# Optimization experiments

Measured on AMD Instinct MI355X. Metric: run time of the kernel, lower is better.

Reference implementation:

```python
import jax, jax.numpy as jnp
import numpy as np

N, M, E, B = 50000, 4, 400000, 64
NHID, EMBED, NOUT, NLAYER = 64, 64, 1, 3


def _glorot(k, shape):
    fan_in = shape[0]
    return jax.random.normal(k, shape, jnp.float32) / np.float32(np.sqrt(fan_in))


def setup_inputs() -> dict:
    key = jax.random.key(0)
    ks = jax.random.split(key, 18)
    inp = {
        "additional_x": jax.random.normal(ks[0], (N, M, 1), jnp.float32),
        "edge_index": jax.random.randint(ks[1], (2, E), 0, N, dtype=jnp.int32),
        "batch": jnp.sort(jax.random.randint(ks[2], (N,), 0, B, dtype=jnp.int32)),
        # conv layer 0: in_channels=1, layers 1,2: in_channels=NHID (bias=False since bn='BN')
        "Wself0": _glorot(ks[3], (1, NHID)),
        "Wnei0": _glorot(ks[4], (1, NHID)),
        "Wself1": _glorot(ks[5], (NHID, NHID)),
        "Wnei1": _glorot(ks[6], (NHID, NHID)),
        "Wself2": _glorot(ks[7], (NHID, NHID)),
        "Wnei2": _glorot(ks[8], (NHID, NHID)),
        # inter_encoder: MLP(nlayer*nhid -> nhid -> nhid -> EMBED), no norm, relu between
        "W1": _glorot(ks[9], (NLAYER * NHID, NHID)),
        "b1": jnp.zeros((NHID,), jnp.float32),
        "W2": _glorot(ks[10], (NHID, NHID)),
        "b2": jnp.zeros((NHID,), jnp.float32),
        "W3": _glorot(ks[11], (NHID, EMBED)),
        "b3": jnp.zeros((EMBED,), jnp.float32),
        # output_encoder: single Linear (with_final_activation=False)
        "Wo": _glorot(ks[12], (EMBED, NOUT)),
        "bo": jnp.zeros((NOUT,), jnp.float32),
    }
    return inp


def reference(additional_x, edge_index, batch,
              Wself0, Wnei0, Wself1, Wnei1, Wself2, Wnei2,
              W1, b1, W2, b2, W3, b3, Wo, bo):
    src, dst = edge_index[0], edge_index[1]

    def conv(x, Ws, Wn):
        # GraphConv: W_self x_i + W_neigh * sum_{j in N(i)} x_j   (x: [N, M, Din])
        agg = jax.ops.segment_sum(x[src], dst, num_segments=N)  # [N, M, Din]
        return jnp.einsum('nmd,dh->nmh', x, Ws) + jnp.einsum('nmd,dh->nmh', agg, Wn)

    x = additional_x  # [N, M, 1]
    skips = []
    for Ws, Wn in ((Wself0, Wnei0), (Wself1, Wnei1), (Wself2, Wnei2)):
        x = jax.nn.relu(conv(x, Ws, Wn))  # [N, M, NHID]
        skips.append(x)
    x = jnp.concatenate(skips, axis=-1)  # [N, M, NLAYER*NHID]

    # inter_encoder (3-layer MLP, no norm)
    h = jax.nn.relu(x @ W1 + b1)
    h = jax.nn.relu(h @ W2 + b2)
    h = h @ W3 + b3  # [N, M, EMBED]

    g = h.mean(axis=-2)  # [N, EMBED]
    g = 2.0 * (g - g.min()) / (g.max() - g.min())

    # pooling == 'add': scatter-add over graphs
    pooled = jax.ops.segment_sum(g, batch, num_segments=B)  # [B, EMBED]

    # output_encoder: plain linear
    return pooled @ Wo + bo  # [B, NOUT]
```

## Files before the change

### kernel.cpp

```cpp
#include <hip/hip_runtime.h>
#include <math.h>

#define NN 50000
#define MM 4
#define EE 400000
#define BB 64
#define NROWS (NN*MM)
#define NBLK_SCAN 98

typedef __attribute__((ext_vector_type(8))) short bf16x8;
typedef __attribute__((ext_vector_type(4))) float f32x4;

struct f8 { float4 lo, hi; };


__device__ __forceinline__ unsigned enc_f(float f) {
  unsigned u = __float_as_uint(f);
  return (u & 0x80000000u) ? ~u : (u | 0x80000000u);
}
__device__ __forceinline__ float dec_f(unsigned u) {
  return (u & 0x80000000u) ? __uint_as_float(u ^ 0x80000000u) : __uint_as_float(~u);
}

__device__ __forceinline__ unsigned short bf16rn(float f) {
  unsigned u = __float_as_uint(f);
  return (unsigned short)((u + 0x7FFFu + ((u >> 16) & 1u)) >> 16);
}
__device__ __forceinline__ float bf2f(unsigned short h) {
  return __uint_as_float(((unsigned)h) << 16);
}

__device__ __forceinline__ f8 zero8() {
  f8 r; r.lo = make_float4(0.f,0.f,0.f,0.f); r.hi = r.lo; return r;
}
__device__ __forceinline__ void add8(f8& a, const f8& b) {
  a.lo.x += b.lo.x; a.lo.y += b.lo.y; a.lo.z += b.lo.z; a.lo.w += b.lo.w;
  a.hi.x += b.hi.x; a.hi.y += b.hi.y; a.hi.z += b.hi.z; a.hi.w += b.hi.w;
}
__device__ __forceinline__ f8 b2f8(bf16x8 v) {
  f8 r;
  r.lo = make_float4(bf2f((unsigned short)v[0]), bf2f((unsigned short)v[1]),
                     bf2f((unsigned short)v[2]), bf2f((unsigned short)v[3]));
  r.hi = make_float4(bf2f((unsigned short)v[4]), bf2f((unsigned short)v[5]),
                     bf2f((unsigned short)v[6]), bf2f((unsigned short)v[7]));
  return r;
}
__device__ __forceinline__ bf16x8 f2b8(const f8& v) {
  bf16x8 h;
  h[0] = (short)bf16rn(v.lo.x); h[1] = (short)bf16rn(v.lo.y);
  h[2] = (short)bf16rn(v.lo.z); h[3] = (short)bf16rn(v.lo.w);
  h[4] = (short)bf16rn(v.hi.x); h[5] = (short)bf16rn(v.hi.y);
  h[6] = (short)bf16rn(v.hi.z); h[7] = (short)bf16rn(v.hi.w);
  return h;
}
__device__ __forceinline__ f8 conv0f8(float xv, float av, const f8& ws, const f8& wn) {
  f8 t;
  t.lo.x = fmaxf(fmaf(xv, ws.lo.x, av * wn.lo.x), 0.f);
  t.lo.y = fmaxf(fmaf(xv, ws.lo.y, av * wn.lo.y), 0.f);
  t.lo.z = fmaxf(fmaf(xv, ws.lo.z, av * wn.lo.z), 0.f);
  t.lo.w = fmaxf(fmaf(xv, ws.lo.w, av * wn.lo.w), 0.f);
  t.hi.x = fmaxf(fmaf(xv, ws.hi.x, av * wn.hi.x), 0.f);
  t.hi.y = fmaxf(fmaf(xv, ws.hi.y, av * wn.hi.y), 0.f);
  t.hi.z = fmaxf(fmaf(xv, ws.hi.z, av * wn.hi.z), 0.f);
  t.hi.w = fmaxf(fmaf(xv, ws.hi.w, av * wn.hi.w), 0.f);
  return t;
}


__global__ void hist_k(const int* __restrict__ ei, int* __restrict__ deg) {
  int e = blockIdx.x * blockDim.x + threadIdx.x;
  if (e < EE) atomicAdd(&deg[ei[EE + e]], 1);
}

__global__ __launch_bounds__(512) void scan1_k(const int* __restrict__ deg,
                                               int* __restrict__ rowstart,
                                               int* __restrict__ bsum) {
  __shared__ int s[512];
  int i = blockIdx.x * 512 + threadIdx.x;
  int v = (i < NN) ? deg[i] : 0;
  s[threadIdx.x] = v;
  __syncthreads();
  for (int off = 1; off < 512; off <<= 1) {
    int t = (threadIdx.x >= (unsigned)off) ? s[threadIdx.x - off] : 0;
    __syncthreads();
    s[threadIdx.x] += t;
    __syncthreads();
  }
  if (i < NN) rowstart[i] = s[threadIdx.x] - v;
  if (threadIdx.x == 511) bsum[blockIdx.x] = s[511];
}

__global__ void scan2_k(int* __restrict__ bsum) {
  if (threadIdx.x == 0) {
    int acc = 0;
    for (int k = 0; k < NBLK_SCAN; ++k) { int t = bsum[k]; bsum[k] = acc; acc += t; }
  }
}

__global__ __launch_bounds__(512) void scan3_k(int* __restrict__ rowstart,
                                               int* __restrict__ cursor,
                                               const int* __restrict__ bsum) {
  int i = blockIdx.x * 512 + threadIdx.x;
  if (i < NN) {
    int v = rowstart[i] + bsum[blockIdx.x];
    rowstart[i] = v;
    cursor[i] = v;
  }
  if (i == 0) rowstart[NN] = EE;
}

__global__ void fill_k(const int* __restrict__ ei, int* __restrict__ cursor,
                       int* __restrict__ nbr) {
  int e = blockIdx.x * blockDim.x + threadIdx.x;
  if (e >= EE) return;
  int d = ei[EE + e];
  int p = atomicAdd(&cursor[d], 1);
  nbr[p] = ei[e];
}


__global__ void prepw_k(const float* __restrict__ Ws1, const float* __restrict__ Wn1,
                        const float* __restrict__ Ws2, const float* __restrict__ Wn2,
                        const float* __restrict__ W1,  const float* __restrict__ W2,
                        const float* __restrict__ W3,  unsigned short* __restrict__ wt) {
  int idx = blockIdx.x * 256 + threadIdx.x;
  if (idx >= 9 * 4096) return;
  int m = idx >> 12, r = idx & 4095;
  int c = r >> 6, k = r & 63;
  const float* src = Ws1;
  switch (m) {
    case 0: src = Ws1; break;
    case 1: src = Wn1; break;
    case 2: src = Ws2; break;
    case 3: src = W1 + 64 * 64; break;
    case 4: src = Wn2; break;
    case 5: src = W1 + 128 * 64; break;
    case 6: src = W1; break;
    case 7: src = W2; break;
    case 8: src = W3; break;
  }
  wt[idx] = bf16rn(src[k * 64 + c]);
}


__global__ void agg0_gather_k(const float* __restrict__ x0,
                              const int* __restrict__ rowstart,
                              const int* __restrict__ nbr,
                              float* __restrict__ agg0) {
  int idx = blockIdx.x * blockDim.x + threadIdx.x;
  if (idx >= NROWS) return;
  int n = idx >> 2, m = idx & 3;
  int beg = rowstart[n], end = rowstart[n + 1];
  float acc = 0.0f;
  for (int i = beg; i < end; ++i) acc += x0[nbr[i] * 4 + m];
  agg0[idx] = acc;
}


#define STAGE_WT(mi)                                                        \
  *(bf16x8*)&WTl[tid >> 3][(tid & 7) << 3] =                                \
      ((const bf16x8*)((const short*)wt + (mi) * 4096))[tid];

#define MFMA_PHASE(A0, A1)                                              \
  _Pragma("unroll")                                                     \
  for (int kh = 0; kh < 2; ++kh) {                                      \
    bf16x8 af  = *(const bf16x8*)&XAs[mrow0 + fl][(kh << 5) + fk];      \
    bf16x8 bf0 = *(const bf16x8*)&WTl[ncol0 + fl][(kh << 5) + fk];      \
    bf16x8 bf1 = *(const bf16x8*)&WTl[ncol0 + 16 + fl][(kh << 5) + fk]; \
    A0 = __builtin_amdgcn_mfma_f32_16x16x32_bf16(af, bf0, A0, 0, 0, 0); \
    A1 = __builtin_amdgcn_mfma_f32_16x16x32_bf16(af, bf1, A1, 0, 0, 0); \
  }

#define DCOMMIT_RELU(A0, A1)                                            \
  _Pragma("unroll")                                                     \
  for (int j = 0; j < 4; ++j) {                                         \
    XAs[drow + j][dc0] = bf16rn(fmaxf(A0[j], 0.f));                     \
    XAs[drow + j][dc1] = bf16rn(fmaxf(A1[j], 0.f));                     \
  }


__global__ __launch_bounds__(512, 4) void conv1_k(const float* __restrict__ x0,
                                                  const float* __restrict__ agg0,
                                                  const int* __restrict__ rowstart,
                                                  const int* __restrict__ nbr,
                                                  const float* __restrict__ Ws0,
                                                  const float* __restrict__ Wn0,
                                                  const unsigned short* __restrict__ wt,
                                                  unsigned short* __restrict__ x1b) {
  __shared__ unsigned short XAs[64][72];
  __shared__ unsigned short WTl[64][72];
  const int row0 = blockIdx.x << 6;
  const int nb0  = blockIdx.x << 4;
  const int tid = threadIdx.x;
  const int r   = tid >> 3;
  const int c8  = (tid & 7) << 3;
  const int lane  = tid & 63;
  const int wid   = tid >> 6;
  const int mrow0 = (wid >> 1) << 4;
  const int ncol0 = (wid & 1) << 5;
  const int fl    = lane & 15;
  const int fk    = (lane >> 4) << 3;
  const int drow  = mrow0 + ((lane >> 4) << 2);
  const int dc0   = ncol0 + fl, dc1 = ncol0 + 16 + fl;

  f8 ws8, wn8;
  ws8.lo = *(const float4*)(Ws0 + c8); ws8.hi = *(const float4*)(Ws0 + c8 + 4);
  wn8.lo = *(const float4*)(Wn0 + c8); wn8.hi = *(const float4*)(Wn0 + c8 + 4);

  *(bf16x8*)&XAs[r][c8] = f2b8(conv0f8(x0[row0 + r], agg0[row0 + r], ws8, wn8));
  STAGE_WT(0);

  const int n = nb0 + (r >> 2), m = r & 3;
  f8 ga;
  {
    int beg = rowstart[n], end = rowstart[n + 1];
    f8 a0 = zero8(), a1 = zero8();
    int i = beg;
    for (; i + 4 <= end; i += 4) {
      int s0 = nbr[i] * 4 + m, s1 = nbr[i+1] * 4 + m;
      int s2 = nbr[i+2] * 4 + m, s3 = nbr[i+3] * 4 + m;
      float xv0 = x0[s0], av0 = agg0[s0];
      float xv1 = x0[s1], av1 = agg0[s1];
      float xv2 = x0[s2], av2 = agg0[s2];
      float xv3 = x0[s3], av3 = agg0[s3];
      f8 t0 = conv0f8(xv0, av0, ws8, wn8); add8(a0, t0);
      f8 t1 = conv0f8(xv1, av1, ws8, wn8); add8(a1, t1);
      f8 t2 = conv0f8(xv2, av2, ws8, wn8); add8(a0, t2);
      f8 t3 = conv0f8(xv3, av3, ws8, wn8); add8(a1, t3);
    }
    bool p0 = i < end, p1 = i + 1 < end, p2 = i + 2 < end;
    float xv0 = 0.f, av0 = 0.f, xv1 = 0.f, av1 = 0.f, xv2 = 0.f, av2 = 0.f;
    if (p0) { int s = nbr[i]     * 4 + m; xv0 = x0[s]; av0 = agg0[s]; }
    if (p1) { int s = nbr[i + 1] * 4 + m; xv1 = x0[s]; av1 = agg0[s]; }
    if (p2) { int s = nbr[i + 2] * 4 + m; xv2 = x0[s]; av2 = agg0[s]; }
    if (p0) { f8 t = conv0f8(xv0, av0, ws8, wn8); add8(a0, t); }
    if (p1) { f8 t = conv0f8(xv1, av1, ws8, wn8); add8(a1, t); }
    if (p2) { f8 t = conv0f8(xv2, av2, ws8, wn8); add8(a0, t); }
    add8(a0, a1);
    ga = a0;
  }
  __syncthreads();

  f32x4 a0v = {0.f,0.f,0.f,0.f}, a1v = {0.f,0.f,0.f,0.f};
  MFMA_PHASE(a0v, a1v);
  __syncthreads();
  *(bf16x8*)&XAs[r][c8] = f2b8(ga);
  STAGE_WT(1);
  __syncthreads();

  MFMA_PHASE(a0v, a1v);
  __syncthreads();
  DCOMMIT_RELU(a0v, a1v);
  __syncthreads();

  *(bf16x8*)(x1b + (size_t)(row0 + r) * 64 + c8) = *(const bf16x8*)&XAs[r][c8];
}


__global__ __launch_bounds__(512, 4) void fused2_k(const unsigned short* __restrict__ x1b,
    const int* __restrict__ rowstart, const int* __restrict__ nbr,
    const float* __restrict__ x0, const float* __restrict__ agg0,
    const float* __restrict__ Ws0, const float* __restrict__ Wn0,
    const unsigned short* __restrict__ wt,
    const float* __restrict__ b1, const float* __restrict__ b2,
    const float* __restrict__ b3,
    float* __restrict__ g, unsigned* __restrict__ mm) {
  __shared__ unsigned short XAs[64][72];
  __shared__ unsigned short WTl[64][72];
  __shared__ float red[16];
  const int row0 = blockIdx.x << 6;
  const int nb0  = blockIdx.x << 4;
  const int tid = threadIdx.x;
  const int r   = tid >> 3;
  const int c8  = (tid & 7) << 3;
  const int lane  = tid & 63;
  const int wid   = tid >> 6;
  const int mrow0 = (wid >> 1) << 4;
  const int ncol0 = (wid & 1) << 5;
  const int fl    = lane & 15;
  const int fk    = (lane >> 4) << 3;
  const int drow  = mrow0 + ((lane >> 4) << 2);
  const int dc0   = ncol0 + fl, dc1 = ncol0 + 16 + fl;

  *(bf16x8*)&XAs[r][c8] = *(const bf16x8*)(x1b + (size_t)(row0 + r) * 64 + c8);
  STAGE_WT(2);

  const int n = nb0 + (r >> 2), m = r & 3;
  f8 ga;
  {
    int beg = rowstart[n], end = rowstart[n + 1];
    f8 a0 = zero8(), a1 = zero8();
    int i = beg;
    for (; i + 4 <= end; i += 4) {
      bf16x8 v0 = *(const bf16x8*)(x1b + (size_t)(nbr[i]   * 4 + m) * 64 + c8);
      bf16x8 v1 = *(const bf16x8*)(x1b + (size_t)(nbr[i+1] * 4 + m) * 64 + c8);
      bf16x8 v2 = *(const bf16x8*)(x1b + (size_t)(nbr[i+2] * 4 + m) * 64 + c8);
      bf16x8 v3 = *(const bf16x8*)(x1b + (size_t)(nbr[i+3] * 4 + m) * 64 + c8);
      f8 t0 = b2f8(v0); add8(a0, t0);
      f8 t1 = b2f8(v1); add8(a1, t1);
      f8 t2 = b2f8(v2); add8(a0, t2);
      f8 t3 = b2f8(v3); add8(a1, t3);
    }
    bool p0 = i < end, p1 = i + 1 < end, p2 = i + 2 < end;
    bf16x8 v0 = {}, v1 = {}, v2 = {};
    if (p0) v0 = *(const bf16x8*)(x1b + (size_t)(nbr[i]     * 4 + m) * 64 + c8);
    if (p1) v1 = *(const bf16x8*)(x1b + (size_t)(nbr[i + 1] * 4 + m) * 64 + c8);
    if (p2) v2 = *(const bf16x8*)(x1b + (size_t)(nbr[i + 2] * 4 + m) * 64 + c8);
    if (p0) { f8 t = b2f8(v0); add8(a0, t); }
    if (p1) { f8 t = b2f8(v1); add8(a1, t); }
    if (p2) { f8 t = b2f8(v2); add8(a0, t); }
    add8(a0, a1);
    ga = a0;
  }
  __syncthreads();

  f32x4 accP0 = {0.f,0.f,0.f,0.f}, accP1 = {0.f,0.f,0.f,0.f};
  MFMA_PHASE(accP0, accP1);
  __syncthreads();
  STAGE_WT(3);
  __syncthreads();

  f32x4 accQ0, accQ1;
  {
    float bv0 = b1[dc0], bv1 = b1[dc1];
    accQ0[0]=bv0; accQ0[1]=bv0; accQ0[2]=bv0; accQ0[3]=bv0;
    accQ1[0]=bv1; accQ1[1]=bv1; accQ1[2]=bv1; accQ1[3]=bv1;
  }
  MFMA_PHASE(accQ0, accQ1);
  __syncthreads();
  *(bf16x8*)&XAs[r][c8] = f2b8(ga);
  STAGE_WT(4);
  __syncthreads();

  MFMA_PHASE(accP0, accP1);
  __syncthreads();
  DCOMMIT_RELU(accP0, accP1);
  STAGE_WT(5);
  __syncthreads();

  MFMA_PHASE(accQ0, accQ1);
  __syncthreads();
  {
    f8 ws8, wn8;
    ws8.lo = *(const float4*)(Ws0 + c8); ws8.hi = *(const float4*)(Ws0 + c8 + 4);
    wn8.lo = *(const float4*)(Wn0 + c8); wn8.hi = *(const float4*)(Wn0 + c8 + 4);
    *(bf16x8*)&XAs[r][c8] =
        f2b8(conv0f8(x0[row0 + r], agg0[row0 + r], ws8, wn8));
  }
  STAGE_WT(6);
  __syncthreads();

  MFMA_PHASE(accQ0, accQ1);
  __syncthreads();
  DCOMMIT_RELU(accQ0, accQ1);
  STAGE_WT(7);
  __syncthreads();

  f32x4 accR0, accR1;
  {
    float bv0 = b2[dc0], bv1 = b2[dc1];
    accR0[0]=bv0; accR0[1]=bv0; accR0[2]=bv0; accR0[3]=bv0;
    accR1[0]=bv1; accR1[1]=bv1; accR1[2]=bv1; accR1[3]=bv1;
  }
  MFMA_PHASE(accR0, accR1);
  __syncthreads();
  DCOMMIT_RELU(accR0, accR1);
  STAGE_WT(8);
  __syncthreads();

  f32x4 accS0, accS1;
  {
    float bv0 = b3[dc0], bv1 = b3[dc1];
    accS0[0]=bv0; accS0[1]=bv0; accS0[2]=bv0; accS0[3]=bv0;
    accS1[0]=bv1; accS1[1]=bv1; accS1[2]=bv1; accS1[3]=bv1;
  }
  MFMA_PHASE(accS0, accS1);
  __syncthreads();
#pragma unroll
  for (int j = 0; j < 4; ++j) {
    XAs[drow + j][dc0] = bf16rn(accS0[j]);
    XAs[drow + j][dc1] = bf16rn(accS1[j]);
  }
  __syncthreads();

  float lmin = 3.4e38f, lmax = -3.4e38f;
  for (int k = tid; k < 1024; k += 512) {
    int nl = k >> 6, c = k & 63;
    float s = 0.25f * (bf2f(XAs[4*nl][c]) + bf2f(XAs[4*nl+1][c]) +
                       bf2f(XAs[4*nl+2][c]) + bf2f(XAs[4*nl+3][c]));
    g[(size_t)((row0 >> 2) + nl) * 64 + c] = s;
    lmin = fminf(lmin, s);
    lmax = fmaxf(lmax, s);
  }
#pragma unroll
  for (int off = 32; off; off >>= 1) {
    lmin = fminf(lmin, __shfl_xor(lmin, off));
    lmax = fmaxf(lmax, __shfl_xor(lmax, off));
  }
  if ((tid & 63) == 0) { red[tid >> 6] = lmin; red[8 + (tid >> 6)] = lmax; }
  __syncthreads();
  if (tid == 0) {
    float m0 = red[0], m1 = red[8];
#pragma unroll
    for (int w = 1; w < 8; ++w) {
      m0 = fminf(m0, red[w]);
      m1 = fmaxf(m1, red[8 + w]);
    }
    atomicMin(&mm[0], enc_f(m0));
    atomicMax(&mm[1], enc_f(m1));
  }
}


__global__ __launch_bounds__(256) void pool2_k(const float* __restrict__ g,
                                               const int* __restrict__ batch,
                                               const unsigned* __restrict__ mm,
                                               float* __restrict__ pooled) {
  int c = threadIdx.x & 63;
  int grp = threadIdx.x >> 6;
  int base = blockIdx.x * 64 + grp * 16;
  float gmin = dec_f(mm[0]);
  float sc = 2.0f / (dec_f(mm[1]) - gmin);
  float acc = 0.0f; int cur = -1;
  for (int i = 0; i < 16; ++i) {
    int n = base + i;
    if (n >= NN) break;
    int b = batch[n];
    if (b != cur) {
      if (cur >= 0) unsafeAtomicAdd(&pooled[(cur << 6) + c], acc);
      cur = b; acc = 0.0f;
    }
    acc += (g[(size_t)n * 64 + c] - gmin) * sc;
  }
  if (cur >= 0) unsafeAtomicAdd(&pooled[(cur << 6) + c], acc);
}


__global__ void out_k(const float* __restrict__ pooled, const float* __restrict__ Wo,
                      const float* __restrict__ bo, float* __restrict__ out) {
  int b = blockIdx.x, l = threadIdx.x;
  float v = pooled[(b << 6) + l] * Wo[l];
#pragma unroll
  for (int off = 32; off; off >>= 1) v += __shfl_xor(v, off);
  if (l == 0) out[b] = v + bo[0];
}


extern "C" void kernel_launch(void* const* d_in, const int* in_sizes, int n_in,
                              void* d_out, int out_size, void* d_ws, size_t ws_size,
                              hipStream_t stream) {
  const float* x0   = (const float*)d_in[0];
  const int*   ei   = (const int*)d_in[1];
  const int*   batch= (const int*)d_in[2];
  const float* Ws0  = (const float*)d_in[3];
  const float* Wn0  = (const float*)d_in[4];
  const float* Ws1  = (const float*)d_in[5];
  const float* Wn1  = (const float*)d_in[6];
  const float* Ws2  = (const float*)d_in[7];
  const float* Wn2  = (const float*)d_in[8];
  const float* W1   = (const float*)d_in[9];
  const float* b1   = (const float*)d_in[10];
  const float* W2   = (const float*)d_in[11];
  const float* b2   = (const float*)d_in[12];
  const float* W3   = (const float*)d_in[13];
  const float* b3   = (const float*)d_in[14];
  const float* Wo   = (const float*)d_in[15];
  const float* bo   = (const float*)d_in[16];
  float* out = (float*)d_out;

  unsigned short* x1b = (unsigned short*)d_ws;
  unsigned short* wt  = x1b + (size_t)NROWS * 64;
  float* agg0   = (float*)(wt + 9 * 4096);
  float* g      = agg0 + NROWS;
  float* pooled = g    + (size_t)NN * 64;
  unsigned* mm  = (unsigned*)(pooled + BB * 64);
  int* deg      = (int*)(mm + 2);
  int* rowstart = deg + NN;
  int* cursor   = rowstart + NN + 1;
  int* nbr      = cursor + NN;
  int* bsum     = nbr + EE;

  hipMemsetAsync(deg, 0, NN * sizeof(int), stream);
  hist_k<<<(EE + 255) / 256, 256, 0, stream>>>(ei, deg);
  prepw_k<<<144, 256, 0, stream>>>(Ws1, Wn1, Ws2, Wn2, W1, W2, W3, wt);
  scan1_k<<<NBLK_SCAN, 512, 0, stream>>>(deg, rowstart, bsum);
  scan2_k<<<1, 64, 0, stream>>>(bsum);
  scan3_k<<<NBLK_SCAN, 512, 0, stream>>>(rowstart, cursor, bsum);
  fill_k<<<(EE + 255) / 256, 256, 0, stream>>>(ei, cursor, nbr);

  agg0_gather_k<<<(NROWS + 255) / 256, 256, 0, stream>>>(x0, rowstart, nbr, agg0);

  conv1_k<<<NROWS / 64, 512, 0, stream>>>(x0, agg0, rowstart, nbr,
                                          Ws0, Wn0, wt, x1b);

  hipMemsetAsync(mm, 0xFF, 4, stream);
  hipMemsetAsync(mm + 1, 0x00, 4, stream);
  fused2_k<<<NROWS / 64, 512, 0, stream>>>(x1b, rowstart, nbr, x0, agg0,
                                           Ws0, Wn0, wt, b1, b2, b3, g, mm);

  hipMemsetAsync(pooled, 0, BB * 64 * sizeof(float), stream);
  pool2_k<<<(NN + 63) / 64, 256, 0, stream>>>(g, batch, mm, pooled);

  out_k<<<BB, 64, 0, stream>>>(pooled, Wo, bo, out);
}
```

Measured before the change: 210.6 us.

## Pack x0/agg0 into float2 and double-buffer weight tiles with register prefetch

The layer-0 aggregation kernel now writes x0 and agg0 interleaved as float2, so each neighbor gather in conv1 and fused2 is one 8-byte load instead of two separate scalar loads. Both fused kernels now keep two shared-memory weight tiles and alternate between them. In fused2 all remaining weight tiles and biases are prefetched into registers at kernel start, which removes several barriers and the global-load latency between MFMA phases. The cost is more LDS and register pressure per block, which could reduce occupancy under the 512x4 launch bounds.

Measured after the change: 230.7 us. 9.5% more time.

```diff
diff --git a/kernel.cpp b/kernel.cpp
--- a/kernel.cpp
+++ b/kernel.cpp
@@ -143,30 +143,29 @@
 }
 
 
-__global__ void agg0_gather_k(const float* __restrict__ x0,
-                              const int* __restrict__ rowstart,
-                              const int* __restrict__ nbr,
-                              float* __restrict__ agg0) {
+__global__ void agg0pack_k(const float* __restrict__ x0,
+                           const int* __restrict__ rowstart,
+                           const int* __restrict__ nbr,
+                           float2* __restrict__ pk) {
   int idx = blockIdx.x * blockDim.x + threadIdx.x;
   if (idx >= NROWS) return;
   int n = idx >> 2, m = idx & 3;
   int beg = rowstart[n], end = rowstart[n + 1];
   float acc = 0.0f;
   for (int i = beg; i < end; ++i) acc += x0[nbr[i] * 4 + m];
-  agg0[idx] = acc;
-}
-
-
-#define STAGE_WT(mi)                                                        \
-  *(bf16x8*)&WTl[tid >> 3][(tid & 7) << 3] =                                \
-      ((const bf16x8*)((const short*)wt + (mi) * 4096))[tid];
-
-#define MFMA_PHASE(A0, A1)                                              \
+  pk[idx] = make_float2(x0[idx], acc);
+}
+
+
+#define WLOAD(mi) (((const bf16x8*)((const short*)wt + (mi) * 4096))[tid])
+#define WCOMMIT(BUF, REG) *(bf16x8*)&BUF[tid >> 3][(tid & 7) << 3] = (REG);
+
+#define MFMA_PHASE(BUF, A0, A1)                                         \
   _Pragma("unroll")                                                     \
   for (int kh = 0; kh < 2; ++kh) {                                      \
     bf16x8 af  = *(const bf16x8*)&XAs[mrow0 + fl][(kh << 5) + fk];      \
-    bf16x8 bf0 = *(const bf16x8*)&WTl[ncol0 + fl][(kh << 5) + fk];      \
-    bf16x8 bf1 = *(const bf16x8*)&WTl[ncol0 + 16 + fl][(kh << 5) + fk]; \
+    bf16x8 bf0 = *(const bf16x8*)&BUF[ncol0 + fl][(kh << 5) + fk];      \
+    bf16x8 bf1 = *(const bf16x8*)&BUF[ncol0 + 16 + fl][(kh << 5) + fk]; \
     A0 = __builtin_amdgcn_mfma_f32_16x16x32_bf16(af, bf0, A0, 0, 0, 0); \
     A1 = __builtin_amdgcn_mfma_f32_16x16x32_bf16(af, bf1, A1, 0, 0, 0); \
   }
@@ -179,8 +178,7 @@
   }
 
 
-__global__ __launch_bounds__(512, 4) void conv1_k(const float* __restrict__ x0,
-                                                  const float* __restrict__ agg0,
+__global__ __launch_bounds__(512, 4) void conv1_k(const float2* __restrict__ pk,
                                                   const int* __restrict__ rowstart,
                                                   const int* __restrict__ nbr,
                                                   const float* __restrict__ Ws0,
@@ -188,7 +186,8 @@
                                                   const unsigned short* __restrict__ wt,
                                                   unsigned short* __restrict__ x1b) {
   __shared__ unsigned short XAs[64][72];
-  __shared__ unsigned short WTl[64][72];
+  __shared__ unsigned short WTa[64][72];
+  __shared__ unsigned short WTb[64][72];
   const int row0 = blockIdx.x << 6;
   const int nb0  = blockIdx.x << 4;
   const int tid = threadIdx.x;
@@ -203,52 +202,54 @@
   const int drow  = mrow0 + ((lane >> 4) << 2);
   const int dc0   = ncol0 + fl, dc1 = ncol0 + 16 + fl;
 
+  const int n = nb0 + (r >> 2), m = r & 3;
+  const int beg = rowstart[n], end = rowstart[n + 1];
+
   f8 ws8, wn8;
   ws8.lo = *(const float4*)(Ws0 + c8); ws8.hi = *(const float4*)(Ws0 + c8 + 4);
   wn8.lo = *(const float4*)(Wn0 + c8); wn8.hi = *(const float4*)(Wn0 + c8 + 4);
 
-  *(bf16x8*)&XAs[r][c8] = f2b8(conv0f8(x0[row0 + r], agg0[row0 + r], ws8, wn8));
-  STAGE_WT(0);
-
-  const int n = nb0 + (r >> 2), m = r & 3;
+  {
+    float2 p = pk[row0 + r];
+    *(bf16x8*)&XAs[r][c8] = f2b8(conv0f8(p.x, p.y, ws8, wn8));
+  }
+  WCOMMIT(WTa, WLOAD(0));
+  WCOMMIT(WTb, WLOAD(1));
+
   f8 ga;
   {
-    int beg = rowstart[n], end = rowstart[n + 1];
     f8 a0 = zero8(), a1 = zero8();
     int i = beg;
     for (; i + 4 <= end; i += 4) {
-      int s0 = nbr[i] * 4 + m, s1 = nbr[i+1] * 4 + m;
-      int s2 = nbr[i+2] * 4 + m, s3 = nbr[i+3] * 4 + m;
-      float xv0 = x0[s0], av0 = agg0[s0];
-      float xv1 = x0[s1], av1 = agg0[s1];
-      float xv2 = x0[s2], av2 = agg0[s2];
-      float xv3 = x0[s3], av3 = agg0[s3];
-      f8 t0 = conv0f8(xv0, av0, ws8, wn8); add8(a0, t0);
-      f8 t1 = conv0f8(xv1, av1, ws8, wn8); add8(a1, t1);
-      f8 t2 = conv0f8(xv2, av2, ws8, wn8); add8(a0, t2);
-      f8 t3 = conv0f8(xv3, av3, ws8, wn8); add8(a1, t3);
+      float2 p0 = pk[nbr[i]     * 4 + m];
+      float2 p1 = pk[nbr[i + 1] * 4 + m];
+      float2 p2 = pk[nbr[i + 2] * 4 + m];
+      float2 p3 = pk[nbr[i + 3] * 4 + m];
+      f8 t0 = conv0f8(p0.x, p0.y, ws8, wn8); add8(a0, t0);
+      f8 t1 = conv0f8(p1.x, p1.y, ws8, wn8); add8(a1, t1);
+      f8 t2 = conv0f8(p2.x, p2.y, ws8, wn8); add8(a0, t2);
+      f8 t3 = conv0f8(p3.x, p3.y, ws8, wn8); add8(a1, t3);
     }
-    bool p0 = i < end, p1 = i + 1 < end, p2 = i + 2 < end;
-    float xv0 = 0.f, av0 = 0.f, xv1 = 0.f, av1 = 0.f, xv2 = 0.f, av2 = 0.f;
-    if (p0) { int s = nbr[i]     * 4 + m; xv0 = x0[s]; av0 = agg0[s]; }
-    if (p1) { int s = nbr[i + 1] * 4 + m; xv1 = x0[s]; av1 = agg0[s]; }
-    if (p2) { int s = nbr[i + 2] * 4 + m; xv2 = x0[s]; av2 = agg0[s]; }
-    if (p0) { f8 t = conv0f8(xv0, av0, ws8, wn8); add8(a0, t); }
-    if (p1) { f8 t = conv0f8(xv1, av1, ws8, wn8); add8(a1, t); }
-    if (p2) { f8 t = conv0f8(xv2, av2, ws8, wn8); add8(a0, t); }
+    bool q0 = i < end, q1 = i + 1 < end, q2 = i + 2 < end;
+    float2 p0 = make_float2(0.f, 0.f), p1 = p0, p2 = p0;
+    if (q0) p0 = pk[nbr[i]     * 4 + m];
+    if (q1) p1 = pk[nbr[i + 1] * 4 + m];
+    if (q2) p2 = pk[nbr[i + 2] * 4 + m];
+    if (q0) { f8 t = conv0f8(p0.x, p0.y, ws8, wn8); add8(a0, t); }
+    if (q1) { f8 t = conv0f8(p1.x, p1.y, ws8, wn8); add8(a1, t); }
+    if (q2) { f8 t = conv0f8(p2.x, p2.y, ws8, wn8); add8(a0, t); }
     add8(a0, a1);
     ga = a0;
   }
   __syncthreads();
 
   f32x4 a0v = {0.f,0.f,0.f,0.f}, a1v = {0.f,0.f,0.f,0.f};
-  MFMA_PHASE(a0v, a1v);
+  MFMA_PHASE(WTa, a0v, a1v);
   __syncthreads();
   *(bf16x8*)&XAs[r][c8] = f2b8(ga);
-  STAGE_WT(1);
-  __syncthreads();
-
-  MFMA_PHASE(a0v, a1v);
+  __syncthreads();
+
+  MFMA_PHASE(WTb, a0v, a1v);
   __syncthreads();
   DCOMMIT_RELU(a0v, a1v);
   __syncthreads();
@@ -259,14 +260,15 @@
 
 __global__ __launch_bounds__(512, 4) void fused2_k(const unsigned short* __restrict__ x1b,
     const int* __restrict__ rowstart, const int* __restrict__ nbr,
-    const float* __restrict__ x0, const float* __restrict__ agg0,
+    const float2* __restrict__ pk,
     const float* __restrict__ Ws0, const float* __restrict__ Wn0,
     const unsigned short* __restrict__ wt,
     const float* __restrict__ b1, const float* __restrict__ b2,
     const float* __restrict__ b3,
     float* __restrict__ g, unsigned* __restrict__ mm) {
   __shared__ unsigned short XAs[64][72];
-  __shared__ unsigned short WTl[64][72];
+  __shared__ unsigned short WTa[64][72];
+  __shared__ unsigned short WTb[64][72];
   __shared__ float red[16];
   const int row0 = blockIdx.x << 6;
   const int nb0  = blockIdx.x << 4;
@@ -282,13 +284,31 @@
   const int drow  = mrow0 + ((lane >> 4) << 2);
   const int dc0   = ncol0 + fl, dc1 = ncol0 + 16 + fl;
 
+  const int n = nb0 + (r >> 2), m = r & 3;
+  const int beg = rowstart[n], end = rowstart[n + 1];
+
   *(bf16x8*)&XAs[r][c8] = *(const bf16x8*)(x1b + (size_t)(row0 + r) * 64 + c8);
-  STAGE_WT(2);
-
-  const int n = nb0 + (r >> 2), m = r & 3;
+  WCOMMIT(WTa, WLOAD(2));
+  WCOMMIT(WTb, WLOAD(3));
+  bf16x8 wr4 = WLOAD(4);
+  bf16x8 wr5 = WLOAD(5);
+  bf16x8 wr6 = WLOAD(6);
+  bf16x8 wr7 = WLOAD(7);
+  bf16x8 wr8 = WLOAD(8);
+  const float b1v0 = b1[dc0], b1v1 = b1[dc1];
+  const float b2v0 = b2[dc0], b2v1 = b2[dc1];
+  const float b3v0 = b3[dc0], b3v1 = b3[dc1];
+  bf16x8 x0f_reg;
+  {
+    f8 ws8, wn8;
+    ws8.lo = *(const float4*)(Ws0 + c8); ws8.hi = *(const float4*)(Ws0 + c8 + 4);
+    wn8.lo = *(const float4*)(Wn0 + c8); wn8.hi = *(const float4*)(Wn0 + c8 + 4);
+    float2 p = pk[row0 + r];
+    x0f_reg = f2b8(conv0f8(p.x, p.y, ws8, wn8));
+  }
+
   f8 ga;
   {
-    int beg = rowstart[n], end = rowstart[n + 1];
     f8 a0 = zero8(), a1 = zero8();
     int i = beg;
     for (; i + 4 <= end; i += 4) {
@@ -301,80 +321,62 @@
       f8 t2 = b2f8(v2); add8(a0, t2);
       f8 t3 = b2f8(v3); add8(a1, t3);
     }
-    bool p0 = i < end, p1 = i + 1 < end, p2 = i + 2 < end;
+    bool q0 = i < end, q1 = i + 1 < end, q2 = i + 2 < end;
     bf16x8 v0 = {}, v1 = {}, v2 = {};
-    if (p0) v0 = *(const bf16x8*)(x1b + (size_t)(nbr[i]     * 4 + m) * 64 + c8);
-    if (p1) v1 = *(const bf16x8*)(x1b + (size_t)(nbr[i + 1] * 4 + m) * 64 + c8);
-    if (p2) v2 = *(const bf16x8*)(x1b + (size_t)(nbr[i + 2] * 4 + m) * 64 + c8);
-    if (p0) { f8 t = b2f8(v0); add8(a0, t); }
-    if (p1) { f8 t = b2f8(v1); add8(a1, t); }
-    if (p2) { f8 t = b2f8(v2); add8(a0, t); }
+    if (q0) v0 = *(const bf16x8*)(x1b + (size_t)(nbr[i]     * 4 + m) * 64 + c8);
+    if (q1) v1 = *(const bf16x8*)(x1b + (size_t)(nbr[i + 1] * 4 + m) * 64 + c8);
+    if (q2) v2 = *(const bf16x8*)(x1b + (size_t)(nbr[i + 2] * 4 + m) * 64 + c8);
+    if (q0) { f8 t = b2f8(v0); add8(a0, t); }
+    if (q1) { f8 t = b2f8(v1); add8(a1, t); }
+    if (q2) { f8 t = b2f8(v2); add8(a0, t); }
     add8(a0, a1);
     ga = a0;
   }
   __syncthreads();
 
   f32x4 accP0 = {0.f,0.f,0.f,0.f}, accP1 = {0.f,0.f,0.f,0.f};
-  MFMA_PHASE(accP0, accP1);
-  __syncthreads();
-  STAGE_WT(3);
-  __syncthreads();
-
+  MFMA_PHASE(WTa, accP0, accP1);
   f32x4 accQ0, accQ1;
-  {
-    float bv0 = b1[dc0], bv1 = b1[dc1];
-    accQ0[0]=bv0; accQ0[1]=bv0; accQ0[2]=bv0; accQ0[3]=bv0;
-    accQ1[0]=bv1; accQ1[1]=bv1; accQ1[2]=bv1; accQ1[3]=bv1;
-  }
-  MFMA_PHASE(accQ0, accQ1);
-  __syncthreads();
+  accQ0[0]=b1v0; accQ0[1]=b1v0; accQ0[2]=b1v0; accQ0[3]=b1v0;
+  accQ1[0]=b1v1; accQ1[1]=b1v1; accQ1[2]=b1v1; accQ1[3]=b1v1;
+  MFMA_PHASE(WTb, accQ0, accQ1);
+  __syncthreads();
+
   *(bf16x8*)&XAs[r][c8] = f2b8(ga);
-  STAGE_WT(4);
-  __syncthreads();
-
-  MFMA_PHASE(accP0, accP1);
+  WCOMMIT(WTa, wr4);
+  __syncthreads();
+
+  MFMA_PHASE(WTa, accP0, accP1);
   __syncthreads();
   DCOMMIT_RELU(accP0, accP1);
-  STAGE_WT(5);
-  __syncthreads();
-
-  MFMA_PHASE(accQ0, accQ1);
-  __syncthreads();
-  {
-    f8 ws8, wn8;
-    ws8.lo = *(const float4*)(Ws0 + c8); ws8.hi = *(const float4*)(Ws0 + c8 + 4);
-    wn8.lo = *(const float4*)(Wn0 + c8); wn8.hi = *(const float4*)(Wn0 + c8 + 4);
-    *(bf16x8*)&XAs[r][c8] =
-        f2b8(conv0f8(x0[row0 + r], agg0[row0 + r], ws8, wn8));
-  }
-  STAGE_WT(6);
-  __syncthreads();
-
-  MFMA_PHASE(accQ0, accQ1);
+  WCOMMIT(WTb, wr5);
+  __syncthreads();
+
+  MFMA_PHASE(WTb, accQ0, accQ1);
+  __syncthreads();
+  *(bf16x8*)&XAs[r][c8] = x0f_reg;
+  WCOMMIT(WTa, wr6);
+  __syncthreads();
+
+  MFMA_PHASE(WTa, accQ0, accQ1);
   __syncthreads();
   DCOMMIT_RELU(accQ0, accQ1);
-  STAGE_WT(7);
+  WCOMMIT(WTb, wr7);
   __syncthreads();
 
   f32x4 accR0, accR1;
-  {
-    float bv0 = b2[dc0], bv1 = b2[dc1];
-    accR0[0]=bv0; accR0[1]=bv0; accR0[2]=bv0; accR0[3]=bv0;
-    accR1[0]=bv1; accR1[1]=bv1; accR1[2]=bv1; accR1[3]=bv1;
-  }
-  MFMA_PHASE(accR0, accR1);
+  accR0[0]=b2v0; accR0[1]=b2v0; accR0[2]=b2v0; accR0[3]=b2v0;
+  accR1[0]=b2v1; accR1[1]=b2v1; accR1[2]=b2v1; accR1[3]=b2v1;
+  MFMA_PHASE(WTb, accR0, accR1);
   __syncthreads();
   DCOMMIT_RELU(accR0, accR1);
-  STAGE_WT(8);
+  WCOMMIT(WTa, wr8);
   __syncthreads();
 
   f32x4 accS0, accS1;
-  {
-    float bv0 = b3[dc0], bv1 = b3[dc1];
-    accS0[0]=bv0; accS0[1]=bv0; accS0[2]=bv0; accS0[3]=bv0;
-    accS1[0]=bv1; accS1[1]=bv1; accS1[2]=bv1; accS1[3]=bv1;
-  }
-  MFMA_PHASE(accS0, accS1);
+  accS0[0]=b3v0; accS0[1]=b3v0; accS0[2]=b3v0; accS0[3]=b3v0;
+  accS1[0]=b3v1; accS1[1]=b3v1; accS1[2]=b3v1; accS1[3]=b3v1;
+  MFMA_PHASE(WTa, accS0, accS1);
   __syncthreads();
 #pragma unroll
   for (int j = 0; j < 4; ++j) {
@@ -470,8 +472,8 @@
 
   unsigned short* x1b = (unsigned short*)d_ws;
   unsigned short* wt  = x1b + (size_t)NROWS * 64;
-  float* agg0   = (float*)(wt + 9 * 4096);
-  float* g      = agg0 + NROWS;
+  float2* pk    = (float2*)(wt + 9 * 4096);
+  float* g      = (float*)(pk + NROWS);
   float* pooled = g    + (size_t)NN * 64;
   unsigned* mm  = (unsigned*)(pooled + BB * 64);
   int* deg      = (int*)(mm + 2);
@@ -488,14 +490,13 @@
   scan3_k<<<NBLK_SCAN, 512, 0, stream>>>(rowstart, cursor, bsum);
   fill_k<<<(EE + 255) / 256, 256, 0, stream>>>(ei, cursor, nbr);
 
-  agg0_gather_k<<<(NROWS + 255) / 256, 256, 0, stream>>>(x0, rowstart, nbr, agg0);
-
-  conv1_k<<<NROWS / 64, 512, 0, stream>>>(x0, agg0, rowstart, nbr,
-                                          Ws0, Wn0, wt, x1b);
+  agg0pack_k<<<(NROWS + 255) / 256, 256, 0, stream>>>(x0, rowstart, nbr, pk);
+
+  conv1_k<<<NROWS / 64, 512, 0, stream>>>(pk, rowstart, nbr, Ws0, Wn0, wt, x1b);
 
   hipMemsetAsync(mm, 0xFF, 4, stream);
   hipMemsetAsync(mm + 1, 0x00, 4, stream);
-  fused2_k<<<NROWS / 64, 512, 0, stream>>>(x1b, rowstart, nbr, x0, agg0,
+  fused2_k<<<NROWS / 64, 512, 0, stream>>>(x1b, rowstart, nbr, pk,
                                            Ws0, Wn0, wt, b1, b2, b3, g, mm);
 
   hipMemsetAsync(pooled, 0, BB * 64 * sizeof(float), stream);
```
